# Kernel optimization log

Measured on AMD Instinct MI355X. Metric: run time of the kernel, lower is better.

The kernel has to match this reference:

```python
import jax, jax.numpy as jnp
import numpy as np

INPUT_CHANNELS = 3

def setup_inputs() -> dict:
    key = jax.random.key(0)
    k1, k2 = jax.random.split(key)
    B, N, C = 16, 4096, 3
    x = jax.random.normal(k1, (B, N, C), dtype=jnp.float32)
    y = jax.random.normal(k2, (B, N, C), dtype=jnp.float32)
    return {"x": x, "y": y}

def reference(x, y):
    # Slice to input_channels (identity here since C == INPUT_CHANNELS)
    x = x[:, :, :INPUT_CHANNELS]
    y = y[:, :, :INPUT_CHANNELS]
    # pdist[b, i, j] = ||x_i||^2 + ||y_j||^2 - 2 x_i . y_j  -> squared euclidean
    x2 = jnp.sum(x * x, axis=-1)  # [B, N]
    y2 = jnp.sum(y * y, axis=-1)  # [B, N]
    zz = jnp.einsum('bic,bjc->bij', x, y)  # [B, N, N]
    pdist = x2[:, :, None] + y2[:, None, :] - 2.0 * zz
    # min over axis 1: nearest x for each y; min over axis 2: nearest y for each x
    loss = jnp.mean(jnp.min(pdist, axis=1)) + jnp.mean(jnp.min(pdist, axis=2))
    return loss
```

## Files before the change

### kernel.cpp

```cpp
#include <hip/hip_runtime.h>
#include <stdint.h>

#define BATCH 16
#define NPTS  4096
#define TOT   (BATCH * NPTS)
#define TWOTOT (2 * TOT)
#define JSEG  8

typedef float f4 __attribute__((ext_vector_type(4)));
typedef float f32x4 __attribute__((ext_vector_type(4)));
typedef short bh8 __attribute__((ext_vector_type(8)));
typedef uint32_t u32;
typedef unsigned short u16;

__device__ __forceinline__ u16 bfr(float f) {
    union { float f; u32 u; } v; v.f = f;
    u32 r = v.u + 0x7FFF + ((v.u >> 16) & 1);
    return (u16)(r >> 16);
}
__device__ __forceinline__ float bfback(u16 h) {
    union { u32 u; float f; } v; v.u = ((u32)h) << 16; return v.f;
}
#define BF16_ONE ((u16)0x3F80)

#define MIN3r(d, a, b, c) \
    asm("v_min3_f32 %0, %1, %2, %3" : "=v"(d) : "v"(a), "v"(b), "v"(c))

__global__ __launch_bounds__(256) void pack_mfma(const float* __restrict__ x,
                                                 const float* __restrict__ y,
                                                 u16* __restrict__ Arec,
                                                 u16* __restrict__ Brec,
                                                 float* __restrict__ out) {
    int idx = blockIdx.x * 256 + threadIdx.x;
    if (idx == 0) out[0] = 0.0f;

    bool isx = idx < TOT;
    int r = isx ? idx : (idx - TOT);
    const float* src = isx ? x : y;
    float a = src[r * 3 + 0];
    float b = src[r * 3 + 1];
    float c = src[r * 3 + 2];
    float s2 = fmaf(a, a, fmaf(b, b, c * c));
    u16 s2h = bfr(s2);
    u16 s2l = bfr(s2 - bfback(s2h));

    union { u16 h[16]; f4 v[2]; } rec;
    if (isx) {
        float ax = -2.0f * a, ay = -2.0f * b, az = -2.0f * c;
        u16 ahx = bfr(ax), ahy = bfr(ay), ahz = bfr(az);
        u16 alx = bfr(ax - bfback(ahx));
        u16 aly = bfr(ay - bfback(ahy));
        u16 alz = bfr(az - bfback(ahz));
        rec.h[0] = ahx;  rec.h[1] = ahy;  rec.h[2] = ahz;
        rec.h[3] = ahx;  rec.h[4] = ahy;  rec.h[5] = ahz;
        rec.h[6] = alx;  rec.h[7] = aly;
        rec.h[8] = alz;  rec.h[9] = s2h;  rec.h[10] = s2l;
        rec.h[11] = BF16_ONE; rec.h[12] = BF16_ONE;
        rec.h[13] = 0; rec.h[14] = 0; rec.h[15] = 0;
        f4* dst = (f4*)(Arec + (size_t)r * 16);
        dst[0] = rec.v[0]; dst[1] = rec.v[1];
    } else {
        u16 yhx = bfr(a), yhy = bfr(b), yhz = bfr(c);
        u16 ylx = bfr(a - bfback(yhx));
        u16 yly = bfr(b - bfback(yhy));
        u16 ylz = bfr(c - bfback(yhz));
        rec.h[0] = yhx;  rec.h[1] = yhy;  rec.h[2] = yhz;
        rec.h[3] = ylx;  rec.h[4] = yly;  rec.h[5] = ylz;
        rec.h[6] = yhx;  rec.h[7] = yhy;
        rec.h[8] = yhz;  rec.h[9] = BF16_ONE; rec.h[10] = BF16_ONE;
        rec.h[11] = s2h; rec.h[12] = s2l;
        rec.h[13] = 0; rec.h[14] = 0; rec.h[15] = 0;
        f4* dst = (f4*)(Brec + (size_t)r * 16);
        dst[0] = rec.v[0]; dst[1] = rec.v[1];
    }
}

#define DSRL(dst, base, imm) \
    asm volatile("ds_read_b128 %0, %1 offset:" imm : "=v"(dst) : "v"(base))

#define WAITL(cnt, slot) do { \
    asm volatile("s_waitcnt lgkmcnt(" cnt ")" : "+v"(slot)); \
    __builtin_amdgcn_sched_barrier(0); \
} while (0)

#define MF8(BB) do { \
    p0 = __builtin_amdgcn_mfma_f32_16x16x32_bf16(af0, BB, zc, 0, 0, 0); \
    p1 = __builtin_amdgcn_mfma_f32_16x16x32_bf16(af1, BB, zc, 0, 0, 0); \
    p2 = __builtin_amdgcn_mfma_f32_16x16x32_bf16(af2, BB, zc, 0, 0, 0); \
    p3 = __builtin_amdgcn_mfma_f32_16x16x32_bf16(af3, BB, zc, 0, 0, 0); \
    p4 = __builtin_amdgcn_mfma_f32_16x16x32_bf16(af4, BB, zc, 0, 0, 0); \
    p5 = __builtin_amdgcn_mfma_f32_16x16x32_bf16(af5, BB, zc, 0, 0, 0); \
    p6 = __builtin_amdgcn_mfma_f32_16x16x32_bf16(af6, BB, zc, 0, 0, 0); \
    p7 = __builtin_amdgcn_mfma_f32_16x16x32_bf16(af7, BB, zc, 0, 0, 0); \
} while (0)

#define EPI1() do { \
    ra0[0]=fminf(ra0[0],p0[0]); ra0[1]=fminf(ra0[1],p0[1]); ra0[2]=fminf(ra0[2],p0[2]); ra0[3]=fminf(ra0[3],p0[3]); \
    ra1[0]=fminf(ra1[0],p1[0]); ra1[1]=fminf(ra1[1],p1[1]); ra1[2]=fminf(ra1[2],p1[2]); ra1[3]=fminf(ra1[3],p1[3]); \
    ra2[0]=fminf(ra2[0],p2[0]); ra2[1]=fminf(ra2[1],p2[1]); ra2[2]=fminf(ra2[2],p2[2]); ra2[3]=fminf(ra2[3],p2[3]); \
    ra3[0]=fminf(ra3[0],p3[0]); ra3[1]=fminf(ra3[1],p3[1]); ra3[2]=fminf(ra3[2],p3[2]); ra3[3]=fminf(ra3[3],p3[3]); \
    ra4[0]=fminf(ra4[0],p4[0]); ra4[1]=fminf(ra4[1],p4[1]); ra4[2]=fminf(ra4[2],p4[2]); ra4[3]=fminf(ra4[3],p4[3]); \
    ra5[0]=fminf(ra5[0],p5[0]); ra5[1]=fminf(ra5[1],p5[1]); ra5[2]=fminf(ra5[2],p5[2]); ra5[3]=fminf(ra5[3],p5[3]); \
    ra6[0]=fminf(ra6[0],p6[0]); ra6[1]=fminf(ra6[1],p6[1]); ra6[2]=fminf(ra6[2],p6[2]); ra6[3]=fminf(ra6[3],p6[3]); \
    ra7[0]=fminf(ra7[0],p7[0]); ra7[1]=fminf(ra7[1],p7[1]); ra7[2]=fminf(ra7[2],p7[2]); ra7[3]=fminf(ra7[3],p7[3]); \
    float t0,t1,t2,t3,t4,t5,t6,t7,t8,t9,t10,u0,u1,u2,u3,cv; \
    MIN3r(t0, p0[0], p0[1], p0[2]); \
    MIN3r(t1, p0[3], p1[0], p1[1]); \
    MIN3r(t2, p1[2], p1[3], p2[0]); \
    MIN3r(t3, p2[1], p2[2], p2[3]); \
    MIN3r(t4, p3[0], p3[1], p3[2]); \
    MIN3r(t5, p3[3], p4[0], p4[1]); \
    MIN3r(t6, p4[2], p4[3], p5[0]); \
    MIN3r(t7, p5[1], p5[2], p5[3]); \
    MIN3r(t8, p6[0], p6[1], p6[2]); \
    MIN3r(t9, p6[3], p7[0], p7[1]); \
    MIN3r(t10, p7[2], p7[3], t0); \
    MIN3r(u0, t1, t2, t3); \
    MIN3r(u1, t4, t5, t6); \
    MIN3r(u2, t7, t8, t9); \
    MIN3r(u3, t10, u0, u1); \
    cv = fminf(u2, u3); \
    asm volatile("ds_min_f32 %0, %1" :: "v"(cma), "v"(cv)); \
    cma += 64; \
} while (0)

__global__ __launch_bounds__(256) void chamfer_mfma(const u16* __restrict__ Arec,
                                                    const u16* __restrict__ Brec,
                                                    float* __restrict__ colpart,
                                                    float* __restrict__ rowpart) {
    constexpr int QLEN = NPTS / JSEG;
    __shared__ u16  Bst[QLEN * 16];
    __shared__ float colmin[QLEN];

    int bid  = blockIdx.x;
    int b    = bid >> 6;
    int ic   = (bid >> 3) & 7;
    int jseg = bid & 7;
    int tid  = threadIdx.x;
    int wv   = tid >> 6, lane = tid & 63;
    int lg   = lane >> 4, lm = lane & 15;

    int i0 = ic * 512 + wv * 128;
    int j0 = jseg * QLEN;

    {
        const f4* src = (const f4*)(Brec + ((size_t)b * NPTS + j0) * 16);
        f4* dst = (f4*)Bst;
        int t4 = tid * 4;
        f4 v0 = src[t4 + 0], v1 = src[t4 + 1], v2 = src[t4 + 2], v3 = src[t4 + 3];
        dst[t4 + 0] = v0; dst[t4 + 1] = v1; dst[t4 + 2] = v2; dst[t4 + 3] = v3;
    }
    for (int i = tid; i < QLEN; i += 256) colmin[i] = 3.4e38f;

    bh8 af0, af1, af2, af3, af4, af5, af6, af7;
    {
        bh8 z8 = {0, 0, 0, 0, 0, 0, 0, 0};
        const u16* ab = Arec + ((size_t)b * NPTS + i0 + lm) * 16 + lg * 8;
        af0 = (lg < 2) ? *(const bh8*)(ab + 0)    : z8;
        af1 = (lg < 2) ? *(const bh8*)(ab + 256)  : z8;
        af2 = (lg < 2) ? *(const bh8*)(ab + 512)  : z8;
        af3 = (lg < 2) ? *(const bh8*)(ab + 768)  : z8;
        af4 = (lg < 2) ? *(const bh8*)(ab + 1024) : z8;
        af5 = (lg < 2) ? *(const bh8*)(ab + 1280) : z8;
        af6 = (lg < 2) ? *(const bh8*)(ab + 1536) : z8;
        af7 = (lg < 2) ? *(const bh8*)(ab + 1792) : z8;
    }
    __syncthreads();

    u32 lofs = (u32)(uintptr_t)&Bst[0] + ((lg < 2) ? (u32)(lm * 32 + lg * 16) : 0u);
    u32 cma  = (u32)(uintptr_t)&colmin[0] + (u32)lm * 4;

    f32x4 zc = {0.f, 0.f, 0.f, 0.f};
    f32x4 big = {3.4e38f, 3.4e38f, 3.4e38f, 3.4e38f};
    f32x4 ra0 = big, ra1 = big, ra2 = big, ra3 = big;
    f32x4 ra4 = big, ra5 = big, ra6 = big, ra7 = big;
    f32x4 p0, p1, p2, p3, p4, p5, p6, p7;
    bh8 s0, s1, s2, s3;

    DSRL(s0, lofs, "0");    DSRL(s1, lofs, "512");
    DSRL(s2, lofs, "1024"); DSRL(s3, lofs, "1536");

    WAITL("3", s0); MF8(s0); DSRL(s0, lofs, "2048"); EPI1();
    WAITL("4", s1); MF8(s1); DSRL(s1, lofs, "2560"); EPI1();
    WAITL("5", s2); MF8(s2); DSRL(s2, lofs, "3072"); EPI1();
    WAITL("6", s3); MF8(s3); DSRL(s3, lofs, "3584"); EPI1();

    u32 lofs2 = lofs + 4096;
    #pragma unroll 1
    for (int k = 0; k < 6; ++k) {
        WAITL("7", s0); MF8(s0); DSRL(s0, lofs2, "0");    EPI1();
        WAITL("7", s1); MF8(s1); DSRL(s1, lofs2, "512");  EPI1();
        WAITL("7", s2); MF8(s2); DSRL(s2, lofs2, "1024"); EPI1();
        WAITL("7", s3); MF8(s3); DSRL(s3, lofs2, "1536"); EPI1();
        lofs2 += 2048;
    }
    WAITL("7", s0); MF8(s0); EPI1();
    WAITL("6", s1); MF8(s1); EPI1();
    WAITL("5", s2); MF8(s2); EPI1();
    WAITL("4", s3); MF8(s3); EPI1();

    #define RRED(r) { r = fminf(r, __shfl_xor(r, 1)); r = fminf(r, __shfl_xor(r, 2)); \
                      r = fminf(r, __shfl_xor(r, 4)); r = fminf(r, __shfl_xor(r, 8)); }
    float* rp = rowpart + (size_t)jseg * TOT + (size_t)b * NPTS + i0 + lg * 4;
    #define RSTORE(pf, fi) do { \
        float a = pf[0], bq = pf[1], c = pf[2], d = pf[3]; \
        RRED(a) RRED(bq) RRED(c) RRED(d) \
        if (lm == 0) { rp[fi*16 + 0] = a; rp[fi*16 + 1] = bq; \
                       rp[fi*16 + 2] = c; rp[fi*16 + 3] = d; } \
    } while (0)
    RSTORE(ra0, 0); RSTORE(ra1, 1); RSTORE(ra2, 2); RSTORE(ra3, 3);
    RSTORE(ra4, 4); RSTORE(ra5, 5); RSTORE(ra6, 6); RSTORE(ra7, 7);

    __syncthreads();
    for (int j = tid; j < QLEN; j += 256)
        colpart[(size_t)ic * TOT + (size_t)b * NPTS + j0 + j] = colmin[j];
}

__global__ __launch_bounds__(256) void chamfer_pass2(const float* __restrict__ rowpart,
                                                     const float* __restrict__ colpart,
                                                     float* __restrict__ out) {
    int t = blockIdx.x * 256 + threadIdx.x;
    float mr = rowpart[t];
    #pragma unroll
    for (int s = 1; s < JSEG; ++s) mr = fminf(mr, rowpart[(size_t)s * TOT + t]);
    float mc = colpart[t];
    #pragma unroll
    for (int ic = 1; ic < 8; ++ic) mc = fminf(mc, colpart[(size_t)ic * TOT + t]);

    float s = mr + mc;
    #pragma unroll
    for (int off = 32; off; off >>= 1) s += __shfl_down(s, off);
    __shared__ float red[4];
    int lane = threadIdx.x & 63, wid = threadIdx.x >> 6;
    if (lane == 0) red[wid] = s;
    __syncthreads();
    if (threadIdx.x == 0) {
        float tot = (red[0] + red[1]) + (red[2] + red[3]);
        atomicAdd(out, tot * (1.0f / (float)TOT));
    }
}

__global__ __launch_bounds__(256) void chamfer_direct(const float* __restrict__ x,
                                                      const float* __restrict__ y,
                                                      float* __restrict__ out) {
    int blk = blockIdx.x;
    int dir = blk >> 8;
    int t = blk & 255;
    int b = t >> 4;
    int chunk = t & 15;
    const float* __restrict__ P = (dir ? y : x) + (b * NPTS + chunk * 256) * 3;
    const float* __restrict__ Q = (dir ? x : y) + b * NPTS * 3;
    float px = P[threadIdx.x * 3 + 0];
    float py = P[threadIdx.x * 3 + 1];
    float pz = P[threadIdx.x * 3 + 2];
    float b0 = 3.4e38f, b1 = 3.4e38f, b2 = 3.4e38f, b3 = 3.4e38f;
    for (int j = 0; j < NPTS; j += 4) {
        #pragma unroll
        for (int u = 0; u < 4; ++u) {
            float dx = px - Q[(j + u) * 3 + 0];
            float dy = py - Q[(j + u) * 3 + 1];
            float dz = pz - Q[(j + u) * 3 + 2];
            float d = fmaf(dx, dx, fmaf(dy, dy, dz * dz));
            if (u == 0) b0 = fminf(b0, d);
            if (u == 1) b1 = fminf(b1, d);
            if (u == 2) b2 = fminf(b2, d);
            if (u == 3) b3 = fminf(b3, d);
        }
    }
    float best = fminf(fminf(b0, b1), fminf(b2, b3));
    float v = best;
    #pragma unroll
    for (int off = 32; off; off >>= 1) v += __shfl_down(v, off);
    __shared__ float red[4];
    int lane = threadIdx.x & 63, wid = threadIdx.x >> 6;
    if (lane == 0) red[wid] = v;
    __syncthreads();
    if (threadIdx.x == 0) {
        float s = (red[0] + red[1]) + (red[2] + red[3]);
        atomicAdd(out, s * (1.0f / (float)TOT));
    }
}

__global__ void zero_kernel(float* out) { out[0] = 0.0f; }

extern "C" void kernel_launch(void* const* d_in, const int* in_sizes, int n_in,
                              void* d_out, int out_size, void* d_ws, size_t ws_size,
                              hipStream_t stream) {
    const float* x = (const float*)d_in[0];
    const float* y = (const float*)d_in[1];
    float* out = (float*)d_out;

    size_t need = (size_t)8 << 20;
    if (ws_size >= need) {
        u16*   Arec    = (u16*)d_ws;
        u16*   Brec    = (u16*)((char*)d_ws + ((size_t)2 << 20));
        float* colpart = (float*)((char*)d_ws + ((size_t)4 << 20));
        float* rowpart = (float*)((char*)d_ws + ((size_t)6 << 20));
        hipLaunchKernelGGL(pack_mfma, dim3(TWOTOT / 256), dim3(256), 0, stream,
                           x, y, Arec, Brec, out);
        hipLaunchKernelGGL(chamfer_mfma, dim3(16 * 8 * JSEG), dim3(256), 0, stream,
                           Arec, Brec, colpart, rowpart);
        hipLaunchKernelGGL(chamfer_pass2, dim3(TOT / 256), dim3(256), 0, stream,
                           rowpart, colpart, out);
    } else {
        hipLaunchKernelGGL(zero_kernel, dim3(1), dim3(1), 0, stream, out);
        hipLaunchKernelGGL(chamfer_direct, dim3(512), dim3(256), 0, stream, x, y, out);
    }
}
```

Baseline: 42.87 us.

## Fuse bf16 record packing into the chamfer MFMA kernel, dropping pack launch

Removes the separate pack kernel and builds the split-bf16 A and B operand records inside the main MFMA kernel, straight from the raw float xyz inputs. This saves one kernel launch and the global write and read-back of the packed records. In exchange each block recomputes the bf16 splits, so packing work is repeated 8x across row and column tiles. The raw 12-byte-stride loads are also less coalesced than the old 16-byte vector loads.

```diff
diff --git a/kernel.cpp b/kernel.cpp
--- a/kernel.cpp
+++ b/kernel.cpp
@@ -4,7 +4,6 @@
 #define BATCH 16
 #define NPTS  4096
 #define TOT   (BATCH * NPTS)
-#define TWOTOT (2 * TOT)
 #define JSEG  8
 
 typedef float f4 __attribute__((ext_vector_type(4)));
@@ -26,53 +25,44 @@
 #define MIN3r(d, a, b, c) \
     asm("v_min3_f32 %0, %1, %2, %3" : "=v"(d) : "v"(a), "v"(b), "v"(c))
 
-__global__ __launch_bounds__(256) void pack_mfma(const float* __restrict__ x,
-                                                 const float* __restrict__ y,
-                                                 u16* __restrict__ Arec,
-                                                 u16* __restrict__ Brec,
-                                                 float* __restrict__ out) {
-    int idx = blockIdx.x * 256 + threadIdx.x;
-    if (idx == 0) out[0] = 0.0f;
-
-    bool isx = idx < TOT;
-    int r = isx ? idx : (idx - TOT);
-    const float* src = isx ? x : y;
-    float a = src[r * 3 + 0];
-    float b = src[r * 3 + 1];
-    float c = src[r * 3 + 2];
+
+__device__ __forceinline__ void build_arec(float a, float b, float c,
+                                           bh8* h0, bh8* h1) {
     float s2 = fmaf(a, a, fmaf(b, b, c * c));
     u16 s2h = bfr(s2);
     u16 s2l = bfr(s2 - bfback(s2h));
-
+    float ax = -2.0f * a, ay = -2.0f * b, az = -2.0f * c;
+    u16 ahx = bfr(ax), ahy = bfr(ay), ahz = bfr(az);
+    u16 alx = bfr(ax - bfback(ahx));
+    u16 aly = bfr(ay - bfback(ahy));
+    u16 alz = bfr(az - bfback(ahz));
+    union { u16 h[8]; bh8 v; } r0, r1;
+    r0.h[0] = ahx; r0.h[1] = ahy; r0.h[2] = ahz;
+    r0.h[3] = ahx; r0.h[4] = ahy; r0.h[5] = ahz;
+    r0.h[6] = alx; r0.h[7] = aly;
+    r1.h[0] = alz; r1.h[1] = s2h; r1.h[2] = s2l;
+    r1.h[3] = BF16_ONE; r1.h[4] = BF16_ONE;
+    r1.h[5] = 0; r1.h[6] = 0; r1.h[7] = 0;
+    *h0 = r0.v; *h1 = r1.v;
+}
+
+__device__ __forceinline__ void build_brec(float a, float b, float c,
+                                           f4* v0, f4* v1) {
+    float s2 = fmaf(a, a, fmaf(b, b, c * c));
+    u16 s2h = bfr(s2);
+    u16 s2l = bfr(s2 - bfback(s2h));
+    u16 yhx = bfr(a), yhy = bfr(b), yhz = bfr(c);
+    u16 ylx = bfr(a - bfback(yhx));
+    u16 yly = bfr(b - bfback(yhy));
+    u16 ylz = bfr(c - bfback(yhz));
     union { u16 h[16]; f4 v[2]; } rec;
-    if (isx) {
-        float ax = -2.0f * a, ay = -2.0f * b, az = -2.0f * c;
-        u16 ahx = bfr(ax), ahy = bfr(ay), ahz = bfr(az);
-        u16 alx = bfr(ax - bfback(ahx));
-        u16 aly = bfr(ay - bfback(ahy));
-        u16 alz = bfr(az - bfback(ahz));
-        rec.h[0] = ahx;  rec.h[1] = ahy;  rec.h[2] = ahz;
-        rec.h[3] = ahx;  rec.h[4] = ahy;  rec.h[5] = ahz;
-        rec.h[6] = alx;  rec.h[7] = aly;
-        rec.h[8] = alz;  rec.h[9] = s2h;  rec.h[10] = s2l;
-        rec.h[11] = BF16_ONE; rec.h[12] = BF16_ONE;
-        rec.h[13] = 0; rec.h[14] = 0; rec.h[15] = 0;
-        f4* dst = (f4*)(Arec + (size_t)r * 16);
-        dst[0] = rec.v[0]; dst[1] = rec.v[1];
-    } else {
-        u16 yhx = bfr(a), yhy = bfr(b), yhz = bfr(c);
-        u16 ylx = bfr(a - bfback(yhx));
-        u16 yly = bfr(b - bfback(yhy));
-        u16 ylz = bfr(c - bfback(yhz));
-        rec.h[0] = yhx;  rec.h[1] = yhy;  rec.h[2] = yhz;
-        rec.h[3] = ylx;  rec.h[4] = yly;  rec.h[5] = ylz;
-        rec.h[6] = yhx;  rec.h[7] = yhy;
-        rec.h[8] = yhz;  rec.h[9] = BF16_ONE; rec.h[10] = BF16_ONE;
-        rec.h[11] = s2h; rec.h[12] = s2l;
-        rec.h[13] = 0; rec.h[14] = 0; rec.h[15] = 0;
-        f4* dst = (f4*)(Brec + (size_t)r * 16);
-        dst[0] = rec.v[0]; dst[1] = rec.v[1];
-    }
+    rec.h[0] = yhx;  rec.h[1] = yhy;  rec.h[2] = yhz;
+    rec.h[3] = ylx;  rec.h[4] = yly;  rec.h[5] = ylz;
+    rec.h[6] = yhx;  rec.h[7] = yhy;
+    rec.h[8] = yhz;  rec.h[9] = BF16_ONE; rec.h[10] = BF16_ONE;
+    rec.h[11] = s2h; rec.h[12] = s2l;
+    rec.h[13] = 0; rec.h[14] = 0; rec.h[15] = 0;
+    *v0 = rec.v[0]; *v1 = rec.v[1];
 }
 
 #define DSRL(dst, base, imm) \
@@ -124,10 +114,11 @@
     cma += 64; \
 } while (0)
 
-__global__ __launch_bounds__(256) void chamfer_mfma(const u16* __restrict__ Arec,
-                                                    const u16* __restrict__ Brec,
+__global__ __launch_bounds__(256) void chamfer_mfma(const float* __restrict__ x,
+                                                    const float* __restrict__ y,
                                                     float* __restrict__ colpart,
-                                                    float* __restrict__ rowpart) {
+                                                    float* __restrict__ rowpart,
+                                                    float* __restrict__ out) {
     constexpr int QLEN = NPTS / JSEG;
     __shared__ u16  Bst[QLEN * 16];
     __shared__ float colmin[QLEN];
@@ -140,30 +131,43 @@
     int wv   = tid >> 6, lane = tid & 63;
     int lg   = lane >> 4, lm = lane & 15;
 
+    if (bid == 0 && tid == 0) out[0] = 0.0f;
+
     int i0 = ic * 512 + wv * 128;
     int j0 = jseg * QLEN;
 
     {
-        const f4* src = (const f4*)(Brec + ((size_t)b * NPTS + j0) * 16);
+        const float* ysrc = y + ((size_t)b * NPTS + j0) * 3;
         f4* dst = (f4*)Bst;
-        int t4 = tid * 4;
-        f4 v0 = src[t4 + 0], v1 = src[t4 + 1], v2 = src[t4 + 2], v3 = src[t4 + 3];
-        dst[t4 + 0] = v0; dst[t4 + 1] = v1; dst[t4 + 2] = v2; dst[t4 + 3] = v3;
+        #pragma unroll
+        for (int r = 0; r < 2; ++r) {
+            int rec = tid * 2 + r;
+            float a = ysrc[rec * 3 + 0];
+            float bb = ysrc[rec * 3 + 1];
+            float c = ysrc[rec * 3 + 2];
+            f4 v0, v1;
+            build_brec(a, bb, c, &v0, &v1);
+            dst[rec * 2 + 0] = v0;
+            dst[rec * 2 + 1] = v1;
+        }
     }
     for (int i = tid; i < QLEN; i += 256) colmin[i] = 3.4e38f;
 
     bh8 af0, af1, af2, af3, af4, af5, af6, af7;
     {
         bh8 z8 = {0, 0, 0, 0, 0, 0, 0, 0};
-        const u16* ab = Arec + ((size_t)b * NPTS + i0 + lm) * 16 + lg * 8;
-        af0 = (lg < 2) ? *(const bh8*)(ab + 0)    : z8;
-        af1 = (lg < 2) ? *(const bh8*)(ab + 256)  : z8;
-        af2 = (lg < 2) ? *(const bh8*)(ab + 512)  : z8;
-        af3 = (lg < 2) ? *(const bh8*)(ab + 768)  : z8;
-        af4 = (lg < 2) ? *(const bh8*)(ab + 1024) : z8;
-        af5 = (lg < 2) ? *(const bh8*)(ab + 1280) : z8;
-        af6 = (lg < 2) ? *(const bh8*)(ab + 1536) : z8;
-        af7 = (lg < 2) ? *(const bh8*)(ab + 1792) : z8;
+        const float* xsrc = x + ((size_t)b * NPTS + i0 + lm) * 3;
+        #define BUILD_AF(af, f) do { \
+            float a = xsrc[f * 48 + 0]; \
+            float bb = xsrc[f * 48 + 1]; \
+            float c = xsrc[f * 48 + 2]; \
+            bh8 h0, h1; \
+            build_arec(a, bb, c, &h0, &h1); \
+            af = (lg == 0) ? h0 : ((lg == 1) ? h1 : z8); \
+        } while (0)
+        BUILD_AF(af0, 0); BUILD_AF(af1, 1); BUILD_AF(af2, 2); BUILD_AF(af3, 3);
+        BUILD_AF(af4, 4); BUILD_AF(af5, 5); BUILD_AF(af6, 6); BUILD_AF(af7, 7);
+        #undef BUILD_AF
     }
     __syncthreads();
 
@@ -290,16 +294,12 @@
     const float* y = (const float*)d_in[1];
     float* out = (float*)d_out;
 
-    size_t need = (size_t)8 << 20;
+    size_t need = (size_t)4 << 20;
     if (ws_size >= need) {
-        u16*   Arec    = (u16*)d_ws;
-        u16*   Brec    = (u16*)((char*)d_ws + ((size_t)2 << 20));
-        float* colpart = (float*)((char*)d_ws + ((size_t)4 << 20));
-        float* rowpart = (float*)((char*)d_ws + ((size_t)6 << 20));
-        hipLaunchKernelGGL(pack_mfma, dim3(TWOTOT / 256), dim3(256), 0, stream,
-                           x, y, Arec, Brec, out);
+        float* colpart = (float*)d_ws;
+        float* rowpart = (float*)((char*)d_ws + ((size_t)2 << 20));
         hipLaunchKernelGGL(chamfer_mfma, dim3(16 * 8 * JSEG), dim3(256), 0, stream,
-                           Arec, Brec, colpart, rowpart);
+                           x, y, colpart, rowpart, out);
         hipLaunchKernelGGL(chamfer_pass2, dim3(TOT / 256), dim3(256), 0, stream,
                            rowpart, colpart, out);
     } else {
```

Result: faster. 38.95 us, median of 2 (-9.1%).
